# Kernel tuning notes

Hardware: AMD Instinct MI355X
Metric: run time of the kernel (lower is better)

Reference implementation:

```python
import jax, jax.numpy as jnp
import numpy as np

HIDDEN = 2048
NUM_HEADS = 16
HEAD_DIM = HIDDEN // NUM_HEADS
ROPE_THETA = 10000.0


def rope_tables(T, dim, base):
    inv_freq = 1.0 / (base ** (jnp.arange(0, dim, 2, dtype=jnp.float32) / dim))
    t = jnp.arange(T, dtype=jnp.float32)
    freqs = jnp.outer(t, inv_freq)              # [T, dim/2]
    emb = jnp.concatenate([freqs, freqs], -1)   # [T, dim]
    return jnp.cos(emb), jnp.sin(emb)


def rotate_half(x):
    x1, x2 = jnp.split(x, 2, axis=-1)
    return jnp.concatenate([-x2, x1], axis=-1)


def setup_inputs() -> dict:
    key = jax.random.key(0)
    ks = jax.random.split(key, 5)
    B, T, C = 2, 2048, HIDDEN
    s = 1.0 / np.sqrt(C)
    return {
        "x": jax.random.normal(ks[0], (B, T, C), jnp.float32),
        "Wq": jax.random.normal(ks[1], (C, C), jnp.float32) * s,
        "Wk": jax.random.normal(ks[2], (C, C), jnp.float32) * s,
        "Wv": jax.random.normal(ks[3], (C, C), jnp.float32) * s,
        "Wo": jax.random.normal(ks[4], (C, C), jnp.float32) * s,
    }


def reference(x, Wq, Wk, Wv, Wo):
    B, T, C = x.shape
    H, D = NUM_HEADS, HEAD_DIM
    scale = D ** -0.5

    # projections (torch Linear: y = x @ W.T)
    q = (x @ Wq.T).reshape(B, T, H, D).transpose(0, 2, 1, 3)  # [B,H,T,D]
    k = (x @ Wk.T).reshape(B, T, H, D).transpose(0, 2, 1, 3)
    v = (x @ Wv.T).reshape(B, T, H, D).transpose(0, 2, 1, 3)

    cos, sin = rope_tables(T, D, ROPE_THETA)  # [T, D]
    cos = cos[None, None, :, :]
    sin = sin[None, None, :, :]
    q = q * cos + rotate_half(q) * sin
    k = k * cos + rotate_half(k) * sin

    scores = jnp.einsum("bhqd,bhkd->bhqk", q, k) * scale
    causal = jnp.tril(jnp.ones((T, T), dtype=bool))
    scores = jnp.where(causal, scores, -jnp.inf)
    probs = jax.nn.softmax(scores, axis=-1)
    out = jnp.einsum("bhqk,bhkd->bhqd", probs, v)
    out = out.transpose(0, 2, 1, 3).reshape(B, T, C)
    return out @ Wo.T
```

## Files before the change

kernel.cpp:

```cpp
#include <hip/hip_runtime.h>
#include <hip/hip_bf16.h>


typedef __attribute__((ext_vector_type(4))) float f32x4;
typedef __attribute__((ext_vector_type(8))) short s16x8;
typedef __attribute__((ext_vector_type(4))) short s16x4;

typedef void __attribute__((address_space(1))) gvoid;
typedef void __attribute__((address_space(3))) svoid;
#define ASYNC16(ldsp, gp) __builtin_amdgcn_global_load_lds((gvoid*)(gp), (svoid*)(ldsp), 16, 0, 0)

__device__ __forceinline__ float bf2f(short b) {
  unsigned u = ((unsigned)(unsigned short)b) << 16;
  float f; __builtin_memcpy(&f, &u, 4); return f;
}
__device__ __forceinline__ short f2bf(float f) {
  unsigned u; __builtin_memcpy(&u, &f, 4);
  u += 0x7FFFu + ((u >> 16) & 1u);
  return (short)(u >> 16);
}

__device__ __forceinline__ f32x4 mfma16(s16x8 a, s16x8 b, f32x4 c) {
  return __builtin_amdgcn_mfma_f32_16x16x32_bf16(a, b, c, 0, 0, 0);
}

__global__ __launch_bounds__(256)
void cvt_k(const float* __restrict__ in, short* __restrict__ out, int n4) {
  int i = blockIdx.x * 256 + threadIdx.x;
  if (i < n4) {
    f32x4 v = *(const f32x4*)&in[i * 4];
    s16x4 o;
#pragma unroll
    for (int e = 0; e < 4; e++) o[e] = f2bf(v[e]);
    *(s16x4*)&out[i * 4] = o;
  }
}

__global__ __launch_bounds__(256)
void cvt_w4_k(const float* __restrict__ w0, const float* __restrict__ w1,
              const float* __restrict__ w2, const float* __restrict__ w3,
              short* __restrict__ o0, short* __restrict__ o1,
              short* __restrict__ o2, short* __restrict__ o3) {
  int i = blockIdx.x * 256 + threadIdx.x;
  int sel = i >> 20, j = i & 1048575;
  const float* in = (sel == 0) ? w0 : (sel == 1) ? w1 : (sel == 2) ? w2 : w3;
  short* out = (sel == 0) ? o0 : (sel == 1) ? o1 : (sel == 2) ? o2 : o3;
  f32x4 v = *(const f32x4*)&in[j * 4];
  s16x4 o;
#pragma unroll
  for (int e = 0; e < 4; e++) o[e] = f2bf(v[e]);
  *(s16x4*)&out[j * 4] = o;
}

__global__ void rope_tables_k(float* __restrict__ cosT, float* __restrict__ sinT) {
  int t = blockIdx.x, j = threadIdx.x;
  float inv = exp2f(-(float)j * 0.20762050593046f);
  float a = (float)t * inv;
  cosT[t * 64 + j] = cosf(a);
  sinT[t * 64 + j] = sinf(a);
}

__global__ __launch_bounds__(256)
void rope_apply_k(short* __restrict__ q, short* __restrict__ kk,
                  const float* __restrict__ cosT, const float* __restrict__ sinT) {
  int gid = blockIdx.x * 256 + threadIdx.x;
  int jb = (gid & 7) * 8;
  int h  = (gid >> 3) & 15;
  int row = gid >> 7;
  int t = row & 2047;
  long base = (long)row * 2048 + h * 128 + jb;
  float cc[8], ss[8];
  *(f32x4*)&cc[0] = *(const f32x4*)&cosT[t * 64 + jb];
  *(f32x4*)&cc[4] = *(const f32x4*)&cosT[t * 64 + jb + 4];
  *(f32x4*)&ss[0] = *(const f32x4*)&sinT[t * 64 + jb];
  *(f32x4*)&ss[4] = *(const f32x4*)&sinT[t * 64 + jb + 4];

  {
    s16x8 lo = *(s16x8*)&q[base];
    s16x8 hi = *(s16x8*)&q[base + 64];
    s16x8 nlo, nhi;
#pragma unroll
    for (int e = 0; e < 8; e++) {
      float a = bf2f(lo[e]), b = bf2f(hi[e]);
      nlo[e] = f2bf(a * cc[e] - b * ss[e]);
      nhi[e] = f2bf(b * cc[e] + a * ss[e]);
    }
    *(s16x8*)&q[base] = nlo;
    *(s16x8*)&q[base + 64] = nhi;
  }
  {
    s16x8 lo = *(s16x8*)&kk[base];
    s16x8 hi = *(s16x8*)&kk[base + 64];
    s16x8 nlo, nhi;
#pragma unroll
    for (int e = 0; e < 8; e++) {
      float a = bf2f(lo[e]), b = bf2f(hi[e]);
      nlo[e] = f2bf(a * cc[e] - b * ss[e]);
      nhi[e] = f2bf(b * cc[e] + a * ss[e]);
    }
    *(s16x8*)&kk[base] = nlo;
    *(s16x8*)&kk[base + 64] = nhi;
  }
}

__device__ __forceinline__ void store_out(float* p, float v) { *p = v; }
__device__ __forceinline__ void store_out(short* p, float v) { *p = f2bf(v); }


#define STAGE_A(Abase, buf, h, t)                                              \
  { ASYNC16(&As[(buf)*16384 + (h)*8192 + lin0*8],                              \
            (Abase) + (long)(m0 + (h)*128 + r0) * K + (t)*64 + kk0);           \
    ASYNC16(&As[(buf)*16384 + (h)*8192 + lin1*8],                              \
            (Abase) + (long)(m0 + (h)*128 + r1) * K + (t)*64 + kk1); }
#define STAGE_B(Bbase, buf, h, t)                                              \
  { ASYNC16(&Bs[(buf)*16384 + (h)*8192 + lin0*8],                              \
            (Bbase) + (long)((h)*128 + r0) * K + (t)*64 + kk0);                \
    ASYNC16(&Bs[(buf)*16384 + (h)*8192 + lin1*8],                              \
            (Bbase) + (long)((h)*128 + r1) * K + (t)*64 + kk1); }
#define LDA(mi, ks) (*(const s16x8*)&As[p*16384 +                              \
    (wr*128 + (mi)*16 + lr)*64 + (((ks)*4 + lk) ^ (lr & 7))*8])
#define LDB(ni, ks) (*(const s16x8*)&Bs[p*16384 +                              \
    (wc*64 + (ni)*16 + lr)*64 + (((ks)*4 + lk) ^ (lr & 7))*8])

template <typename OutT>
__device__ __forceinline__ void gemm8_tile(const short* __restrict__ A,
                                           const short* __restrict__ B,
                                           OutT* __restrict__ Cmat,
                                           int n0, int K, int ldc,
                                           short* As, short* Bs) {
  const int tid = threadIdx.x;
  const int wid = tid >> 6, lane = tid & 63;
  const int lr = lane & 15, lk = lane >> 4;
  const int wr = wid >> 2, wc = wid & 3;
  const int m0 = blockIdx.y * 256;

  const int lin0 = wid * 128 + lane;
  const int lin1 = wid * 128 + 64 + lane;
  const int r0 = lin0 >> 3, r1 = lin1 >> 3;
  const int kk0 = ((lin0 & 7) ^ (r0 & 7)) * 8;
  const int kk1 = ((lin1 & 7) ^ (r1 & 7)) * 8;

  f32x4 acc[8][4] = {};
  const int NT = K >> 6;

  STAGE_A(A, 0, 0, 0); STAGE_A(A, 0, 1, 0);
  STAGE_B(B, 0, 0, 0); STAGE_B(B, 0, 1, 0);
  STAGE_A(A, 1, 0, 1);
  asm volatile("s_waitcnt vmcnt(2)" ::: "memory");
  __builtin_amdgcn_sched_barrier(0);
  __builtin_amdgcn_s_barrier();

  for (int t = 0; t < NT; ++t) {
    const int p = t & 1;
    const bool s1 = (t + 1 < NT), s2 = (t + 2 < NT);
    s16x8 af[8], b0, b1;
#pragma unroll
    for (int mi = 0; mi < 8; mi++) af[mi] = LDA(mi, 0);
    b0 = LDB(0, 0); b1 = LDB(1, 0);
    if (s1) STAGE_A(A, p ^ 1, 1, t + 1);
    __builtin_amdgcn_s_barrier();
    __builtin_amdgcn_s_setprio(1);
#pragma unroll
    for (int mi = 0; mi < 8; mi++) {
      acc[mi][0] = mfma16(af[mi], b0, acc[mi][0]);
      acc[mi][1] = mfma16(af[mi], b1, acc[mi][1]);
    }
    __builtin_amdgcn_s_setprio(0);
    __builtin_amdgcn_s_barrier();
    b0 = LDB(2, 0); b1 = LDB(3, 0);
    if (s1) STAGE_B(B, p ^ 1, 0, t + 1);
    __builtin_amdgcn_s_barrier();
    __builtin_amdgcn_s_setprio(1);
#pragma unroll
    for (int mi = 0; mi < 8; mi++) {
      acc[mi][2] = mfma16(af[mi], b0, acc[mi][2]);
      acc[mi][3] = mfma16(af[mi], b1, acc[mi][3]);
    }
    __builtin_amdgcn_s_setprio(0);
    __builtin_amdgcn_s_barrier();
#pragma unroll
    for (int mi = 0; mi < 8; mi++) af[mi] = LDA(mi, 1);
    b0 = LDB(0, 1); b1 = LDB(1, 1);
    if (s1) STAGE_B(B, p ^ 1, 1, t + 1);
    __builtin_amdgcn_s_barrier();
    __builtin_amdgcn_s_setprio(1);
#pragma unroll
    for (int mi = 0; mi < 8; mi++) {
      acc[mi][0] = mfma16(af[mi], b0, acc[mi][0]);
      acc[mi][1] = mfma16(af[mi], b1, acc[mi][1]);
    }
    __builtin_amdgcn_s_setprio(0);
    __builtin_amdgcn_s_barrier();
    b0 = LDB(2, 1); b1 = LDB(3, 1);
    if (s2) {
      STAGE_A(A, p, 0, t + 2);
      asm volatile("s_waitcnt vmcnt(2)" ::: "memory");
    } else {
      asm volatile("s_waitcnt vmcnt(0)" ::: "memory");
    }
    __builtin_amdgcn_sched_barrier(0);
    __builtin_amdgcn_s_barrier();
    __builtin_amdgcn_s_setprio(1);
#pragma unroll
    for (int mi = 0; mi < 8; mi++) {
      acc[mi][2] = mfma16(af[mi], b0, acc[mi][2]);
      acc[mi][3] = mfma16(af[mi], b1, acc[mi][3]);
    }
    __builtin_amdgcn_s_setprio(0);
    __builtin_amdgcn_s_barrier();
  }
#pragma unroll
  for (int mi = 0; mi < 8; mi++)
#pragma unroll
    for (int ni = 0; ni < 4; ni++)
#pragma unroll
      for (int r = 0; r < 4; r++) {
        int row = m0 + wr * 128 + mi * 16 + lk * 4 + r;
        int col = n0 + wc * 64 + ni * 16 + lr;
        store_out(&Cmat[(long)row * ldc + col], acc[mi][ni][r]);
      }
}

__global__ __launch_bounds__(512, 2)
void gemm8_qkv_k(const short* __restrict__ A,
                 const short* __restrict__ Bq, const short* __restrict__ Bk,
                 const short* __restrict__ Bv,
                 short* __restrict__ Cq, short* __restrict__ Ck,
                 short* __restrict__ Cv, int K) {
  __shared__ short As[2 * 16384];
  __shared__ short Bs[2 * 16384];
  int sel = blockIdx.x >> 3;
  int ncol = (blockIdx.x & 7) * 256;
  const short* B = (sel == 0) ? Bq : (sel == 1) ? Bk : Bv;
  short* C = (sel == 0) ? Cq : (sel == 1) ? Ck : Cv;
  gemm8_tile<short>(A, B + (long)ncol * K, C, ncol, K, 2048, As, Bs);
}

__global__ __launch_bounds__(512, 2)
void gemm8_out_k(const short* __restrict__ A, const short* __restrict__ B,
                 float* __restrict__ C, int K) {
  __shared__ short As[2 * 16384];
  __shared__ short Bs[2 * 16384];
  int ncol = blockIdx.x * 256;
  gemm8_tile<float>(A, B + (long)ncol * K, C, ncol, K, 2048, As, Bs);
}

__global__ __launch_bounds__(256)
void attn_k(const short* __restrict__ q, const short* __restrict__ k,
            const short* __restrict__ v, short* __restrict__ o) {
  __shared__ short Ks[2][64 * 128];
  __shared__ short Vt[128 * 72];
  __shared__ short Pl[4][16 * 72];
  const int tid = threadIdx.x;
  const int wave = tid >> 6, lane = tid & 63;
  const int lr = lane & 15, lq = lane >> 4;
  const int h = blockIdx.y, b = blockIdx.z;
  const long rowb = (long)b * 2048;
  const int hoff = h * 128;
  const float scale = 0.08838834764831845f;

  const int vr = (tid & 31) * 2;
  const int vcol = (tid >> 5) * 16;

  for (int pass = 0; pass < 2; pass++) {
    const int qt = pass ? (31 - blockIdx.x) : blockIdx.x;
    const int qbase = qt * 64;
    const int nt = qt + 1;

    s16x8 qf[4];
    {
      const short* qp = q + (rowb + qbase + wave * 16 + lr) * 2048 + hoff + lq * 8;
#pragma unroll
      for (int ks = 0; ks < 4; ks++) qf[ks] = *(const s16x8*)(qp + ks * 32);
    }
    f32x4 acc[8] = {};
    float mrun[4], lrun[4];
#pragma unroll
    for (int r = 0; r < 4; r++) { mrun[r] = -1e30f; lrun[r] = 0.f; }

    s16x8 vl[4];
    {
      const short* vp = v + (rowb + vr) * 2048 + hoff + vcol;
      vl[0] = *(const s16x8*)vp;       vl[1] = *(const s16x8*)(vp + 8);
      vl[2] = *(const s16x8*)(vp + 2048); vl[3] = *(const s16x8*)(vp + 2048 + 8);
    }
#pragma unroll
    for (int L = 0; L < 4; L++) {
      int ci = L * 256 + tid;
      int krow = ci >> 4, dslot = ci & 15;
      int col = (dslot ^ (krow & 7)) * 8;
      ASYNC16(&Ks[0][ci * 8], k + (rowb + krow) * 2048 + hoff + col);
    }
#pragma unroll
    for (int e = 0; e < 16; e++) {
      int col = vcol + e;
      unsigned pk = (unsigned)(unsigned short)vl[e >> 3][e & 7]
                  | ((unsigned)(unsigned short)vl[2 + (e >> 3)][e & 7] << 16);
      *(unsigned*)&Vt[col * 72 + vr] = pk;
    }
    __syncthreads();

    int cur = 0;
    for (int ti = 0; ti < nt; ti++) {
      const int kv0 = ti * 64;
      const bool pre = (ti + 1 < nt);
      s16x8 vn[4];
      if (pre) {
        const short* vp = v + (rowb + kv0 + 64 + vr) * 2048 + hoff + vcol;
        vn[0] = *(const s16x8*)vp;       vn[1] = *(const s16x8*)(vp + 8);
        vn[2] = *(const s16x8*)(vp + 2048); vn[3] = *(const s16x8*)(vp + 2048 + 8);
#pragma unroll
        for (int L = 0; L < 4; L++) {
          int ci = L * 256 + tid;
          int krow = ci >> 4, dslot = ci & 15;
          int col = (dslot ^ (krow & 7)) * 8;
          ASYNC16(&Ks[cur ^ 1][ci * 8], k + (rowb + kv0 + 64 + krow) * 2048 + hoff + col);
        }
      }
      f32x4 s[4] = {};
#pragma unroll
      for (int kvf = 0; kvf < 4; kvf++) {
        const int krow = kvf * 16 + lr;
#pragma unroll
        for (int ks = 0; ks < 4; ks++) {
          int doff = ks * 4 + lq;
          s16x8 kf = *(const s16x8*)&Ks[cur][krow * 128 + ((doff ^ (krow & 7)) * 8)];
          s[kvf] = mfma16(qf[ks], kf, s[kvf]);
        }
      }
#pragma unroll
      for (int kvf = 0; kvf < 4; kvf++)
#pragma unroll
        for (int r = 0; r < 4; r++) s[kvf][r] *= scale;
      if (ti == nt - 1) {
#pragma unroll
        for (int kvf = 0; kvf < 4; kvf++) {
          int kvc = kv0 + kvf * 16 + lr;
#pragma unroll
          for (int r = 0; r < 4; r++) {
            int qr = qbase + wave * 16 + lq * 4 + r;
            if (kvc > qr) s[kvf][r] = -3.0e38f;
          }
        }
      }
      float mt[4], rs[4];
#pragma unroll
      for (int r = 0; r < 4; r++)
        mt[r] = fmaxf(fmaxf(s[0][r], s[1][r]), fmaxf(s[2][r], s[3][r]));
#pragma unroll
      for (int d = 1; d < 16; d <<= 1)
#pragma unroll
        for (int r = 0; r < 4; r++) mt[r] = fmaxf(mt[r], __shfl_xor(mt[r], d));
      int need = 0;
#pragma unroll
      for (int r = 0; r < 4; r++) need |= (mt[r] > mrun[r] + 8.f);
      if (__any(need)) {
#pragma unroll
        for (int r = 0; r < 4; r++) {
          float mn = fmaxf(mrun[r], mt[r]);
          float sf = __expf(mrun[r] - mn);
          mrun[r] = mn;
          lrun[r] *= sf;
#pragma unroll
          for (int df = 0; df < 8; df++) acc[df][r] *= sf;
        }
      }
      short* pw = &Pl[wave][0];
#pragma unroll
      for (int r = 0; r < 4; r++) rs[r] = 0.f;
#pragma unroll
      for (int kvf = 0; kvf < 4; kvf++)
#pragma unroll
        for (int r = 0; r < 4; r++) {
          float p = __expf(s[kvf][r] - mrun[r]);
          rs[r] += p;
          pw[(lq * 4 + r) * 72 + kvf * 16 + lr] = f2bf(p);
        }
#pragma unroll
      for (int d = 1; d < 16; d <<= 1)
#pragma unroll
        for (int r = 0; r < 4; r++) rs[r] += __shfl_xor(rs[r], d);
#pragma unroll
      for (int r = 0; r < 4; r++) lrun[r] += rs[r];
      s16x8 pf0 = *(const s16x8*)&pw[lr * 72 + lq * 8];
      s16x8 pf1 = *(const s16x8*)&pw[lr * 72 + 32 + lq * 8];
#pragma unroll
      for (int df = 0; df < 8; df++) {
        s16x8 vf0 = *(const s16x8*)&Vt[(df * 16 + lr) * 72 + lq * 8];
        s16x8 vf1 = *(const s16x8*)&Vt[(df * 16 + lr) * 72 + 32 + lq * 8];
        acc[df] = mfma16(pf0, vf0, acc[df]);
        acc[df] = mfma16(pf1, vf1, acc[df]);
      }
      __syncthreads();
      if (pre) {
#pragma unroll
        for (int e = 0; e < 16; e++) {
          int col = vcol + e;
          unsigned pk = (unsigned)(unsigned short)vn[e >> 3][e & 7]
                      | ((unsigned)(unsigned short)vn[2 + (e >> 3)][e & 7] << 16);
          *(unsigned*)&Vt[col * 72 + vr] = pk;
        }
        __syncthreads();
      }
      cur ^= 1;
    }
#pragma unroll
    for (int r = 0; r < 4; r++) {
      float inv = 1.0f / lrun[r];
      long orow = rowb + qbase + wave * 16 + lq * 4 + r;
#pragma unroll
      for (int df = 0; df < 8; df++)
        o[orow * 2048 + hoff + df * 16 + lr] = f2bf(acc[df][r] * inv);
    }
  }
}

extern "C" void kernel_launch(void* const* d_in, const int* in_sizes, int n_in,
                              void* d_out, int out_size, void* d_ws, size_t ws_size,
                              hipStream_t stream) {
  const float* x  = (const float*)d_in[0];
  const float* Wq = (const float*)d_in[1];
  const float* Wk = (const float*)d_in[2];
  const float* Wv = (const float*)d_in[3];
  const float* Wo = (const float*)d_in[4];
  float* out = (float*)d_out;

  char* p = (char*)d_ws;
  short* xb  = (short*)p; p += 8388608L * 2;
  short* wqb = (short*)p; p += 4194304L * 2;
  short* wkb = (short*)p; p += 4194304L * 2;
  short* wvb = (short*)p; p += 4194304L * 2;
  short* wob = (short*)p; p += 4194304L * 2;
  short* qb  = (short*)p; p += 8388608L * 2;
  short* kb  = (short*)p; p += 8388608L * 2;
  short* vb  = (short*)p; p += 8388608L * 2;
  short* ab  = (short*)p; p += 8388608L * 2;
  float* cosT = (float*)p; p += 131072L * 4;
  float* sinT = (float*)p; p += 131072L * 4;

  cvt_k<<<8192, 256, 0, stream>>>(x, xb, 2097152);
  cvt_w4_k<<<16384, 256, 0, stream>>>(Wq, Wk, Wv, Wo, wqb, wkb, wvb, wob);
  rope_tables_k<<<2048, 64, 0, stream>>>(cosT, sinT);

  gemm8_qkv_k<<<dim3(24, 16), 512, 0, stream>>>(xb, wqb, wkb, wvb, qb, kb, vb, 2048);

  rope_apply_k<<<2048, 256, 0, stream>>>(qb, kb, cosT, sinT);

  attn_k<<<dim3(16, 16, 2), 256, 0, stream>>>(qb, kb, vb, ab);

  gemm8_out_k<<<dim3(8, 16), 512, 0, stream>>>(ab, wob, out, 2048);
}
```

Measured before the change: 434.1 us.

## Fuse RoPE and softmax scale into QKV GEMM epilogue, retile output GEMM

```diff
diff --git a/kernel.cpp b/kernel.cpp
--- a/kernel.cpp
+++ b/kernel.cpp
@@ -9,6 +9,7 @@
 typedef void __attribute__((address_space(1))) gvoid;
 typedef void __attribute__((address_space(3))) svoid;
 #define ASYNC16(ldsp, gp) __builtin_amdgcn_global_load_lds((gvoid*)(gp), (svoid*)(ldsp), 16, 0, 0)
+#define VMW(N) asm volatile("s_waitcnt vmcnt(" #N ")" ::: "memory")
 
 __device__ __forceinline__ float bf2f(short b) {
   unsigned u = ((unsigned)(unsigned short)b) << 16;
@@ -25,26 +26,20 @@
 }
 
 __global__ __launch_bounds__(256)
-void cvt_k(const float* __restrict__ in, short* __restrict__ out, int n4) {
+void cvt_all_k(const float* __restrict__ x,
+               const float* __restrict__ w0, const float* __restrict__ w1,
+               const float* __restrict__ w2, const float* __restrict__ w3,
+               short* __restrict__ xb,
+               short* __restrict__ o0, short* __restrict__ o1,
+               short* __restrict__ o2, short* __restrict__ o3) {
   int i = blockIdx.x * 256 + threadIdx.x;
-  if (i < n4) {
-    f32x4 v = *(const f32x4*)&in[i * 4];
-    s16x4 o;
-#pragma unroll
-    for (int e = 0; e < 4; e++) o[e] = f2bf(v[e]);
-    *(s16x4*)&out[i * 4] = o;
+  const float* in; short* out; int j;
+  if (i < 2097152) { in = x; out = xb; j = i; }
+  else {
+    int k2 = i - 2097152; int sel = k2 >> 20; j = k2 & 1048575;
+    in  = (sel == 0) ? w0 : (sel == 1) ? w1 : (sel == 2) ? w2 : w3;
+    out = (sel == 0) ? o0 : (sel == 1) ? o1 : (sel == 2) ? o2 : o3;
   }
-}
-
-__global__ __launch_bounds__(256)
-void cvt_w4_k(const float* __restrict__ w0, const float* __restrict__ w1,
-              const float* __restrict__ w2, const float* __restrict__ w3,
-              short* __restrict__ o0, short* __restrict__ o1,
-              short* __restrict__ o2, short* __restrict__ o3) {
-  int i = blockIdx.x * 256 + threadIdx.x;
-  int sel = i >> 20, j = i & 1048575;
-  const float* in = (sel == 0) ? w0 : (sel == 1) ? w1 : (sel == 2) ? w2 : w3;
-  short* out = (sel == 0) ? o0 : (sel == 1) ? o1 : (sel == 2) ? o2 : o3;
   f32x4 v = *(const f32x4*)&in[j * 4];
   s16x4 o;
 #pragma unroll
@@ -52,101 +47,69 @@
   *(s16x4*)&out[j * 4] = o;
 }
 
-__global__ void rope_tables_k(float* __restrict__ cosT, float* __restrict__ sinT) {
-  int t = blockIdx.x, j = threadIdx.x;
+__global__ __launch_bounds__(256)
+void rope_tables_k(float* __restrict__ cosT, float* __restrict__ sinT) {
+  int id = blockIdx.x * 256 + threadIdx.x;
+  int j = id >> 11, t = id & 2047;
   float inv = exp2f(-(float)j * 0.20762050593046f);
   float a = (float)t * inv;
-  cosT[t * 64 + j] = cosf(a);
-  sinT[t * 64 + j] = sinf(a);
-}
-
-__global__ __launch_bounds__(256)
-void rope_apply_k(short* __restrict__ q, short* __restrict__ kk,
-                  const float* __restrict__ cosT, const float* __restrict__ sinT) {
-  int gid = blockIdx.x * 256 + threadIdx.x;
-  int jb = (gid & 7) * 8;
-  int h  = (gid >> 3) & 15;
-  int row = gid >> 7;
-  int t = row & 2047;
-  long base = (long)row * 2048 + h * 128 + jb;
-  float cc[8], ss[8];
-  *(f32x4*)&cc[0] = *(const f32x4*)&cosT[t * 64 + jb];
-  *(f32x4*)&cc[4] = *(const f32x4*)&cosT[t * 64 + jb + 4];
-  *(f32x4*)&ss[0] = *(const f32x4*)&sinT[t * 64 + jb];
-  *(f32x4*)&ss[4] = *(const f32x4*)&sinT[t * 64 + jb + 4];
-
-  {
-    s16x8 lo = *(s16x8*)&q[base];
-    s16x8 hi = *(s16x8*)&q[base + 64];
-    s16x8 nlo, nhi;
-#pragma unroll
-    for (int e = 0; e < 8; e++) {
-      float a = bf2f(lo[e]), b = bf2f(hi[e]);
-      nlo[e] = f2bf(a * cc[e] - b * ss[e]);
-      nhi[e] = f2bf(b * cc[e] + a * ss[e]);
-    }
-    *(s16x8*)&q[base] = nlo;
-    *(s16x8*)&q[base + 64] = nhi;
-  }
-  {
-    s16x8 lo = *(s16x8*)&kk[base];
-    s16x8 hi = *(s16x8*)&kk[base + 64];
-    s16x8 nlo, nhi;
-#pragma unroll
-    for (int e = 0; e < 8; e++) {
-      float a = bf2f(lo[e]), b = bf2f(hi[e]);
-      nlo[e] = f2bf(a * cc[e] - b * ss[e]);
-      nhi[e] = f2bf(b * cc[e] + a * ss[e]);
-    }
-    *(s16x8*)&kk[base] = nlo;
-    *(s16x8*)&kk[base + 64] = nhi;
-  }
-}
-
-__device__ __forceinline__ void store_out(float* p, float v) { *p = v; }
-__device__ __forceinline__ void store_out(short* p, float v) { *p = f2bf(v); }
-
-
-#define STAGE_A(Abase, buf, h, t)                                              \
-  { ASYNC16(&As[(buf)*16384 + (h)*8192 + lin0*8],                              \
-            (Abase) + (long)(m0 + (h)*128 + r0) * K + (t)*64 + kk0);           \
-    ASYNC16(&As[(buf)*16384 + (h)*8192 + lin1*8],                              \
-            (Abase) + (long)(m0 + (h)*128 + r1) * K + (t)*64 + kk1); }
-#define STAGE_B(Bbase, buf, h, t)                                              \
-  { ASYNC16(&Bs[(buf)*16384 + (h)*8192 + lin0*8],                              \
-            (Bbase) + (long)((h)*128 + r0) * K + (t)*64 + kk0);                \
-    ASYNC16(&Bs[(buf)*16384 + (h)*8192 + lin1*8],                              \
-            (Bbase) + (long)((h)*128 + r1) * K + (t)*64 + kk1); }
-#define LDA(mi, ks) (*(const s16x8*)&As[p*16384 +                              \
-    (wr*128 + (mi)*16 + lr)*64 + (((ks)*4 + lk) ^ (lr & 7))*8])
-#define LDB(ni, ks) (*(const s16x8*)&Bs[p*16384 +                              \
-    (wc*64 + (ni)*16 + lr)*64 + (((ks)*4 + lk) ^ (lr & 7))*8])
-
-template <typename OutT>
-__device__ __forceinline__ void gemm8_tile(const short* __restrict__ A,
-                                           const short* __restrict__ B,
-                                           OutT* __restrict__ Cmat,
-                                           int n0, int K, int ldc,
-                                           short* As, short* Bs) {
+  cosT[j * 2048 + t] = cosf(a);
+  sinT[j * 2048 + t] = sinf(a);
+}
+
+__global__ __launch_bounds__(512, 1)
+void gemm_qkv9_k(const short* __restrict__ A,
+                 const short* __restrict__ Bq, const short* __restrict__ Bk,
+                 const short* __restrict__ Bv,
+                 short* __restrict__ Cq, short* __restrict__ Ck,
+                 short* __restrict__ Cv,
+                 const float* __restrict__ cosT, const float* __restrict__ sinT) {
+  const int K = 2048, NT = 32;
+  __shared__ short As[2 * 16384];
+  __shared__ short Bs[2 * 16384];
   const int tid = threadIdx.x;
   const int wid = tid >> 6, lane = tid & 63;
   const int lr = lane & 15, lk = lane >> 4;
   const int wr = wid >> 2, wc = wid & 3;
+  const int sel = blockIdx.x >> 3;
+  const int n0 = (blockIdx.x & 7) * 256;
   const int m0 = blockIdx.y * 256;
+  const short* B = (sel == 0) ? Bq : (sel == 1) ? Bk : Bv;
+  short* C = (sel == 0) ? Cq : (sel == 1) ? Ck : Cv;
+  const int rope = (sel < 2);
 
   const int lin0 = wid * 128 + lane;
   const int lin1 = wid * 128 + 64 + lane;
   const int r0 = lin0 >> 3, r1 = lin1 >> 3;
   const int kk0 = ((lin0 & 7) ^ (r0 & 7)) * 8;
   const int kk1 = ((lin1 & 7) ^ (r1 & 7)) * 8;
+  auto permrow = [&](int sr) -> int {
+    if (!rope) return sr;
+    int u = sr & 127;
+    return (sr & ~127) | ((u & 1) << 6) | (u >> 1);
+  };
 
   f32x4 acc[8][4] = {};
-  const int NT = K >> 6;
-
-  STAGE_A(A, 0, 0, 0); STAGE_A(A, 0, 1, 0);
-  STAGE_B(B, 0, 0, 0); STAGE_B(B, 0, 1, 0);
-  STAGE_A(A, 1, 0, 1);
-  asm volatile("s_waitcnt vmcnt(2)" ::: "memory");
+
+#define STAGE_A(buf, h, t)                                                     \
+  { ASYNC16(&As[(buf)*16384 + (h)*8192 + lin0*8],                              \
+            A + (long)(m0 + (h)*128 + r0) * K + (t)*64 + kk0);                 \
+    ASYNC16(&As[(buf)*16384 + (h)*8192 + lin1*8],                              \
+            A + (long)(m0 + (h)*128 + r1) * K + (t)*64 + kk1); }
+#define STAGE_B(buf, h, t)                                                     \
+  { ASYNC16(&Bs[(buf)*16384 + (h)*8192 + lin0*8],                              \
+            B + (long)(n0 + permrow((h)*128 + r0)) * K + (t)*64 + kk0);        \
+    ASYNC16(&Bs[(buf)*16384 + (h)*8192 + lin1*8],                              \
+            B + (long)(n0 + permrow((h)*128 + r1)) * K + (t)*64 + kk1); }
+#define LDA(mi, ks) (*(const s16x8*)&As[p*16384 +                              \
+    (wr*128 + (mi)*16 + lr)*64 + (((ks)*4 + lk) ^ (lr & 7))*8])
+#define LDB(ni, ks) (*(const s16x8*)&Bs[p*16384 +                              \
+    (wc*64 + (ni)*16 + lr)*64 + (((ks)*4 + lk) ^ (lr & 7))*8])
+
+  STAGE_A(0, 0, 0); STAGE_A(0, 1, 0);
+  STAGE_B(0, 0, 0); STAGE_B(0, 1, 0);
+  STAGE_A(1, 0, 1);
+  VMW(2);
   __builtin_amdgcn_sched_barrier(0);
   __builtin_amdgcn_s_barrier();
 
@@ -157,7 +120,7 @@
 #pragma unroll
     for (int mi = 0; mi < 8; mi++) af[mi] = LDA(mi, 0);
     b0 = LDB(0, 0); b1 = LDB(1, 0);
-    if (s1) STAGE_A(A, p ^ 1, 1, t + 1);
+    if (s1) { STAGE_A(p ^ 1, 1, t + 1); STAGE_B(p ^ 1, 0, t + 1); STAGE_B(p ^ 1, 1, t + 1); }
     __builtin_amdgcn_s_barrier();
     __builtin_amdgcn_s_setprio(1);
 #pragma unroll
@@ -168,7 +131,6 @@
     __builtin_amdgcn_s_setprio(0);
     __builtin_amdgcn_s_barrier();
     b0 = LDB(2, 0); b1 = LDB(3, 0);
-    if (s1) STAGE_B(B, p ^ 1, 0, t + 1);
     __builtin_amdgcn_s_barrier();
     __builtin_amdgcn_s_setprio(1);
 #pragma unroll
@@ -181,7 +143,6 @@
 #pragma unroll
     for (int mi = 0; mi < 8; mi++) af[mi] = LDA(mi, 1);
     b0 = LDB(0, 1); b1 = LDB(1, 1);
-    if (s1) STAGE_B(B, p ^ 1, 1, t + 1);
     __builtin_amdgcn_s_barrier();
     __builtin_amdgcn_s_setprio(1);
 #pragma unroll
@@ -193,10 +154,10 @@
     __builtin_amdgcn_s_barrier();
     b0 = LDB(2, 1); b1 = LDB(3, 1);
     if (s2) {
-      STAGE_A(A, p, 0, t + 2);
-      asm volatile("s_waitcnt vmcnt(2)" ::: "memory");
+      STAGE_A(p, 0, t + 2);
+      VMW(2);
     } else {
-      asm volatile("s_waitcnt vmcnt(0)" ::: "memory");
+      VMW(0);
     }
     __builtin_amdgcn_sched_barrier(0);
     __builtin_amdgcn_s_barrier();
@@ -209,40 +170,128 @@
     __builtin_amdgcn_s_setprio(0);
     __builtin_amdgcn_s_barrier();
   }
-#pragma unroll
-  for (int mi = 0; mi < 8; mi++)
+  VMW(0);
+  const float qscale = (sel == 0) ? 0.08838834764831845f : 1.0f;
+#pragma unroll
+  for (int mi = 0; mi < 8; mi++) {
+    const int rowb = m0 + wr * 128 + mi * 16 + lk * 4;
+    const int t0 = rowb & 2047;
+#pragma unroll
+    for (int ni = 0; ni < 4; ni++) {
+      const int col = n0 + wc * 64 + ni * 16 + lr;
+      if (rope) {
+        const int j = (wc & 1) * 32 + ni * 8 + (lr >> 1);
+        f32x4 cc = *(const f32x4*)&cosT[j * 2048 + t0];
+        f32x4 sn = *(const f32x4*)&sinT[j * 2048 + t0];
+#pragma unroll
+        for (int r = 0; r < 4; r++) {
+          float a = acc[mi][ni][r];
+          float bpart = __shfl_xor(a, 1);
+          float v = (lr & 1) ? (a * cc[r] + bpart * sn[r])
+                             : (a * cc[r] - bpart * sn[r]);
+          C[(long)(rowb + r) * 2048 + col] = f2bf(v * qscale);
+        }
+      } else {
+#pragma unroll
+        for (int r = 0; r < 4; r++)
+          C[(long)(rowb + r) * 2048 + col] = f2bf(acc[mi][ni][r]);
+      }
+    }
+  }
+#undef STAGE_A
+#undef STAGE_B
+#undef LDA
+#undef LDB
+}
+
+__global__ __launch_bounds__(512, 1)
+void gemm_out9_k(const short* __restrict__ A, const short* __restrict__ Bw,
+                 float* __restrict__ C) {
+  const int K = 2048, NT = 32;
+  __shared__ short As[2 * 16384];
+  __shared__ short Bs[2 * 8192];
+  const int tid = threadIdx.x;
+  const int wid = tid >> 6, lane = tid & 63;
+  const int lr = lane & 15, lk = lane >> 4;
+  const int wr = wid >> 1, wc = wid & 1;
+  const int n0 = blockIdx.x * 128;
+  const int m0 = blockIdx.y * 256;
+  const short* PA = A + (long)m0 * K;
+  const short* PB = Bw + (long)n0 * K;
+
+  f32x4 acc[4][4] = {};
+
+  auto STGO = [&](int buf, int t) {
+    const long kof = (long)t * 64;
+#pragma unroll
+    for (int i = 0; i < 4; i++) {
+      int g = tid + 512 * i, rr = g >> 3;
+      int kk2 = ((g & 7) ^ (rr & 7)) * 8;
+      ASYNC16(&As[buf * 16384 + g * 8], PA + (long)rr * K + kof + kk2);
+    }
+#pragma unroll
+    for (int i = 0; i < 2; i++) {
+      int g = tid + 512 * i, rr = g >> 3;
+      int kk2 = ((g & 7) ^ (rr & 7)) * 8;
+      ASYNC16(&Bs[buf * 8192 + g * 8], PB + (long)rr * K + kof + kk2);
+    }
+  };
+#define LDAO(mi, ks) (*(const s16x8*)&As[p*16384 +                             \
+    (wr*64 + (mi)*16 + lr)*64 + (((ks)*4 + lk) ^ (lr & 7))*8])
+#define LDBO(ni, ks) (*(const s16x8*)&Bs[p*8192 +                              \
+    (wc*64 + (ni)*16 + lr)*64 + (((ks)*4 + lk) ^ (lr & 7))*8])
+
+  STGO(0, 0);
+  VMW(0);
+  __builtin_amdgcn_sched_barrier(0);
+  __builtin_amdgcn_s_barrier();
+
+  for (int t = 0; t < NT; ++t) {
+    const int p = t & 1;
+    const bool s1 = (t + 1 < NT);
+    s16x8 af[4], bf[4];
+#pragma unroll
+    for (int mi = 0; mi < 4; mi++) af[mi] = LDAO(mi, 0);
+#pragma unroll
+    for (int ni = 0; ni < 4; ni++) bf[ni] = LDBO(ni, 0);
+    if (s1) STGO(p ^ 1, t + 1);
+    __builtin_amdgcn_s_barrier();
+    __builtin_amdgcn_s_setprio(1);
+#pragma unroll
+    for (int mi = 0; mi < 4; mi++)
+#pragma unroll
+      for (int ni = 0; ni < 4; ni++)
+        acc[mi][ni] = mfma16(af[mi], bf[ni], acc[mi][ni]);
+    __builtin_amdgcn_s_setprio(0);
+    __builtin_amdgcn_s_barrier();
+#pragma unroll
+    for (int mi = 0; mi < 4; mi++) af[mi] = LDAO(mi, 1);
+#pragma unroll
+    for (int ni = 0; ni < 4; ni++) bf[ni] = LDBO(ni, 1);
+    __builtin_amdgcn_s_barrier();
+    __builtin_amdgcn_s_setprio(1);
+#pragma unroll
+    for (int mi = 0; mi < 4; mi++)
+#pragma unroll
+      for (int ni = 0; ni < 4; ni++)
+        acc[mi][ni] = mfma16(af[mi], bf[ni], acc[mi][ni]);
+    __builtin_amdgcn_s_setprio(0);
+    VMW(0);
+    __builtin_amdgcn_sched_barrier(0);
+    __builtin_amdgcn_s_barrier();
+  }
+#pragma unroll
+  for (int mi = 0; mi < 4; mi++)
 #pragma unroll
     for (int ni = 0; ni < 4; ni++)
 #pragma unroll
       for (int r = 0; r < 4; r++) {
-        int row = m0 + wr * 128 + mi * 16 + lk * 4 + r;
+        int row = m0 + wr * 64 + mi * 16 + lk * 4 + r;
         int col = n0 + wc * 64 + ni * 16 + lr;
-        store_out(&Cmat[(long)row * ldc + col], acc[mi][ni][r]);
-      }
-}
-
-__global__ __launch_bounds__(512, 2)
-void gemm8_qkv_k(const short* __restrict__ A,
-                 const short* __restrict__ Bq, const short* __restrict__ Bk,
-                 const short* __restrict__ Bv,
-                 short* __restrict__ Cq, short* __restrict__ Ck,
-                 short* __restrict__ Cv, int K) {
-  __shared__ short As[2 * 16384];
-  __shared__ short Bs[2 * 16384];
-  int sel = blockIdx.x >> 3;
-  int ncol = (blockIdx.x & 7) * 256;
-  const short* B = (sel == 0) ? Bq : (sel == 1) ? Bk : Bv;
-  short* C = (sel == 0) ? Cq : (sel == 1) ? Ck : Cv;
-  gemm8_tile<short>(A, B + (long)ncol * K, C, ncol, K, 2048, As, Bs);
-}
-
-__global__ __launch_bounds__(512, 2)
-void gemm8_out_k(const short* __restrict__ A, const short* __restrict__ B,
-                 float* __restrict__ C, int K) {
-  __shared__ short As[2 * 16384];
-  __shared__ short Bs[2 * 16384];
-  int ncol = blockIdx.x * 256;
-  gemm8_tile<float>(A, B + (long)ncol * K, C, ncol, K, 2048, As, Bs);
+        C[(long)row * 2048 + col] = acc[mi][ni][r];
+      }
+#undef LDAO
+#undef LDBO
 }
 
 __global__ __launch_bounds__(256)
@@ -257,7 +306,6 @@
   const int h = blockIdx.y, b = blockIdx.z;
   const long rowb = (long)b * 2048;
   const int hoff = h * 128;
-  const float scale = 0.08838834764831845f;
 
   const int vr = (tid & 31) * 2;
   const int vcol = (tid >> 5) * 16;
@@ -328,10 +376,6 @@
           s[kvf] = mfma16(qf[ks], kf, s[kvf]);
         }
       }
-#pragma unroll
-      for (int kvf = 0; kvf < 4; kvf++)
-#pragma unroll
-        for (int r = 0; r < 4; r++) s[kvf][r] *= scale;
       if (ti == nt - 1) {
 #pragma unroll
         for (int kvf = 0; kvf < 4; kvf++) {
@@ -372,9 +416,9 @@
       for (int kvf = 0; kvf < 4; kvf++)
 #pragma unroll
         for (int r = 0; r < 4; r++) {
-          float p = __expf(s[kvf][r] - mrun[r]);
-          rs[r] += p;
-          pw[(lq * 4 + r) * 72 + kvf * 16 + lr] = f2bf(p);
+          float pp = __expf(s[kvf][r] - mrun[r]);
+          rs[r] += pp;
+          pw[(lq * 4 + r) * 72 + kvf * 16 + lr] = f2bf(pp);
         }
 #pragma unroll
       for (int d = 1; d < 16; d <<= 1)
@@ -438,15 +482,13 @@
   float* cosT = (float*)p; p += 131072L * 4;
   float* sinT = (float*)p; p += 131072L * 4;
 
-  cvt_k<<<8192, 256, 0, stream>>>(x, xb, 2097152);
-  cvt_w4_k<<<16384, 256, 0, stream>>>(Wq, Wk, Wv, Wo, wqb, wkb, wvb, wob);
-  rope_tables_k<<<2048, 64, 0, stream>>>(cosT, sinT);
-
-  gemm8_qkv_k<<<dim3(24, 16), 512, 0, stream>>>(xb, wqb, wkb, wvb, qb, kb, vb, 2048);
-
-  rope_apply_k<<<2048, 256, 0, stream>>>(qb, kb, cosT, sinT);
+  cvt_all_k<<<24576, 256, 0, stream>>>(x, Wq, Wk, Wv, Wo, xb, wqb, wkb, wvb, wob);
+  rope_tables_k<<<512, 256, 0, stream>>>(cosT, sinT);
+
+  gemm_qkv9_k<<<dim3(24, 16), 512, 0, stream>>>(xb, wqb, wkb, wvb,
+                                                qb, kb, vb, cosT, sinT);
 
   attn_k<<<dim3(16, 16, 2), 256, 0, stream>>>(qb, kb, vb, ab);
 
-  gemm8_out_k<<<dim3(8, 16), 512, 0, stream>>>(ab, wob, out, 2048);
-}
+  gemm_out9_k<<<dim3(16, 16), 512, 0, stream>>>(ab, wob, out);
+}
```

Measured after the change: 427.5 us. About the same (-1.5%).
